# Kernel optimization log

Hardware: AMD Instinct MI355X
Metric: run time of the kernel (lower is better)

Reference implementation:

```python
import jax, jax.numpy as jnp
import numpy as np

N_NODES = 100000
N_EDGES = 1500000
N_REL = 3
HID = 256


def setup_inputs() -> dict:
    key = jax.random.key(0)
    ks = jax.random.split(key, 8)
    return {
        "feat_a": jax.random.normal(ks[0], (N_NODES, 256), dtype=jnp.float32),
        "feat_b": jax.random.normal(ks[1], (N_NODES, 384), dtype=jnp.float32),
        "Wp_a": jax.random.normal(ks[2], (256, HID), dtype=jnp.float32) * 0.03,
        "Wp_b": jax.random.normal(ks[3], (384, HID), dtype=jnp.float32) * 0.03,
        "Wr": jax.random.normal(ks[4], (N_REL, HID, HID), dtype=jnp.float32) * 0.06,
        "ln_gamma": jnp.ones((HID,), dtype=jnp.float32),
        "ln_beta": jnp.zeros((HID,), dtype=jnp.float32),
        "edge_weight": jax.random.uniform(ks[5], (N_EDGES,), dtype=jnp.float32),
        "edge_src": jax.random.randint(ks[6], (N_EDGES,), 0, N_NODES, dtype=jnp.int32),
        "edge_dst": jax.random.randint(ks[7], (N_EDGES,), 0, N_NODES, dtype=jnp.int32),
    }


def _layer_norm(x, gamma, beta, eps=1e-5):
    mu = jnp.mean(x, axis=-1, keepdims=True)
    var = jnp.mean(jnp.square(x - mu), axis=-1, keepdims=True)
    return (x - mu) * jax.lax.rsqrt(var + eps) * gamma + beta


def reference(feat_a, feat_b, Wp_a, Wp_b, Wr, ln_gamma, ln_beta,
              edge_weight, edge_src, edge_dst):
    # avg fusion of modality projections (bias-free linears), padding node zeroed
    h0 = 0.5 * (feat_a @ Wp_a + feat_b @ Wp_b)  # [N, H]
    h0 = h0.at[0].set(0.0)

    n = h0.shape[0]
    e_per_rel = edge_src.shape[0] // N_REL  # edges pre-sorted by relation id
    aggregated = jnp.zeros_like(h0)
    for r in range(N_REL):
        s = slice(r * e_per_rel, (r + 1) * e_per_rel)
        src, dst, w = edge_src[s], edge_dst[s], edge_weight[s]
        # gather -> relation linear -> weight scale  [E_r, H]
        msg = (h0[src] @ Wr[r]) * w[:, None]
        num = jax.ops.segment_sum(msg, dst, num_segments=n)
        den = jax.ops.segment_sum(w, dst, num_segments=n)
        aggregated = aggregated + num / jnp.maximum(den, 1e-8)[:, None]

    # dropout p=0 / eval -> identity; residual + LayerNorm, padding node zeroed
    h1 = _layer_norm(h0 + aggregated, ln_gamma, ln_beta)
    h1 = h1.at[0].set(0.0)
    return h1
```

## Files before the change

### kernel.cpp

```cpp
#include <hip/hip_runtime.h>

#define N_NODES 100000
#define HID 256
#define N_EDGES 1500000
#define N_REL 3
#define E_PER_REL (N_EDGES / N_REL)
#define NKEYS (N_REL * N_NODES)
#define KP 640
#define KR 768

#define SCAN_CHUNK 1024
#define NSCANBLK ((NKEYS + SCAN_CHUNK - 1) / SCAN_CHUNK)

typedef __attribute__((ext_vector_type(8))) short bf16x8;
typedef __attribute__((ext_vector_type(4))) float f32x4;

__device__ __forceinline__ short f2bf(float x) {
    union { float f; unsigned u; } v; v.f = x;
    unsigned r = v.u + 0x7fffu + ((v.u >> 16) & 1u);
    return (short)(r >> 16);
}
__device__ __forceinline__ float bf2f(short h) {
    union { unsigned u; float f; } v;
    v.u = ((unsigned)(unsigned short)h) << 16;
    return v.f;
}
__device__ __forceinline__ int xorf(int r) { return (r & 3) ^ ((r >> 2) & 3); }

__device__ __forceinline__ void gload16(const void* g, void* l) {
    typedef const __attribute__((address_space(1))) unsigned int gq;
    typedef __attribute__((address_space(3))) unsigned int lq;
    __builtin_amdgcn_global_load_lds((gq*)g, (lq*)l, 16, 0, 0);
}

__global__ __launch_bounds__(256) void wprep_kernel(
    const float* __restrict__ Wa, const float* __restrict__ Wb,
    const float* __restrict__ Wr,
    short* __restrict__ WTp, short* __restrict__ WTr)
{
    int idx = blockIdx.x * 256 + threadIdx.x;
    if (idx < 256 * KP) {
        int c = idx / KP, k = idx - c * KP;
        float v = (k < 256) ? Wa[k * HID + c] : Wb[(k - 256) * HID + c];
        WTp[idx] = f2bf(0.5f * v);
    } else {
        int j = idx - 256 * KP;
        if (j < 256 * KR) {
            int c = j / KR, k = j - c * KR;
            WTr[j] = f2bf(Wr[(k >> 8) * HID * HID + (k & 255) * HID + c]);
        }
    }
}

__global__ __launch_bounds__(512, 2) void proj_gemm(
    const float* __restrict__ fa, const float* __restrict__ fb,
    const short* __restrict__ WTp, short* __restrict__ h0h,
    unsigned char* __restrict__ h0q, float* __restrict__ h0scale)
{
    __shared__ alignas(16) char lds[98304];
    const int tid = threadIdx.x;
    const int lane = tid & 63;
    const int w = tid >> 6;
    const int wr = w >> 2, wc = w & 3;
    const int brow = blockIdx.x * 128;

    auto bufA = [&](int b) -> char* { return lds + b * 32768; };
    auto bufB = [&](int b) -> char* { return lds + b * 32768 + 16384; };

    f32x4 acc[4][4] = {};

    const int a_r8 = lane >> 3;
    const int a_sl = (lane & 7) ^ a_r8;
    int aRowG[2];
    #pragma unroll
    for (int ii = 0; ii < 2; ++ii) {
        int i = w * 2 + ii;
        int gr = brow + i * 8 + a_r8;
        aRowG[ii] = (gr < N_NODES) ? gr : (N_NODES - 1);
    }
    const int b_c16 = lane >> 2;
    int bColL[2], bSl[2];
    #pragma unroll
    for (int ii = 0; ii < 2; ++ii) {
        int i = w * 2 + ii;
        bColL[ii] = i * 16 + b_c16;
        bSl[ii] = (lane & 3) ^ xorf(bColL[ii]);
    }

    auto stage = [&](int b, int k0) {
        const float* asrc; int astr, kk;
        if (k0 < 256) { asrc = fa; astr = 256; kk = k0; }
        else          { asrc = fb; astr = 384; kk = k0 - 256; }
        #pragma unroll
        for (int ii = 0; ii < 2; ++ii) {
            int i = w * 2 + ii;
            gload16(asrc + (size_t)aRowG[ii] * astr + kk + a_sl * 4,
                    bufA(b) + i * 1024);
        }
        #pragma unroll
        for (int ii = 0; ii < 2; ++ii) {
            int i = w * 2 + ii;
            gload16(WTp + (size_t)bColL[ii] * KP + k0 + bSl[ii] * 8,
                    bufB(b) + i * 1024);
        }
    };

    const int nt = KP / 32;
    stage(0, 0); stage(1, 32); stage(2, 64);
    int cur = 0;
    for (int t = 0; t < nt; ++t) {
        if (t < nt - 2)       asm volatile("s_waitcnt vmcnt(8)" ::: "memory");
        else if (t == nt - 2) asm volatile("s_waitcnt vmcnt(4)" ::: "memory");
        else                  asm volatile("s_waitcnt vmcnt(0)" ::: "memory");
        __builtin_amdgcn_s_barrier();

        bf16x8 afr[4], bfr[4];
        #pragma unroll
        for (int m = 0; m < 4; ++m) {
            int rt = wr * 64 + m * 16 + (lane & 15);
            int p0 = (((lane >> 4) << 1) | 0) ^ (rt & 7);
            int p1 = (((lane >> 4) << 1) | 1) ^ (rt & 7);
            f32x4 lo = *(const f32x4*)(bufA(cur) + rt * 128 + p0 * 16);
            f32x4 hi = *(const f32x4*)(bufA(cur) + rt * 128 + p1 * 16);
            union { bf16x8 h; unsigned u[4]; } cv;
            asm("v_cvt_pk_bf16_f32 %0, %1, %2" : "=v"(cv.u[0]) : "v"(lo.x), "v"(lo.y));
            asm("v_cvt_pk_bf16_f32 %0, %1, %2" : "=v"(cv.u[1]) : "v"(lo.z), "v"(lo.w));
            asm("v_cvt_pk_bf16_f32 %0, %1, %2" : "=v"(cv.u[2]) : "v"(hi.x), "v"(hi.y));
            asm("v_cvt_pk_bf16_f32 %0, %1, %2" : "=v"(cv.u[3]) : "v"(hi.z), "v"(hi.w));
            afr[m] = cv.h;
        }
        #pragma unroll
        for (int n = 0; n < 4; ++n) {
            int ct = wc * 64 + n * 16 + (lane & 15);
            int p = (lane >> 4) ^ xorf(ct);
            bfr[n] = *(const bf16x8*)(bufB(cur) + ct * 64 + p * 16);
        }
        #pragma unroll
        for (int m = 0; m < 4; ++m)
            #pragma unroll
            for (int n = 0; n < 4; ++n)
                acc[m][n] = __builtin_amdgcn_mfma_f32_16x16x32_bf16(
                    afr[m], bfr[n], acc[m][n], 0, 0, 0);

        asm volatile("s_waitcnt lgkmcnt(0)" ::: "memory");
        __builtin_amdgcn_sched_barrier(0);
        __builtin_amdgcn_s_barrier();
        if (t + 3 < nt) stage(cur, (t + 3) * 32);
        cur = (cur == 2) ? 0 : cur + 1;
    }

    float* redM  = (float*)lds;
    float* smInv = redM + 512;
    #pragma unroll
    for (int m = 0; m < 4; ++m) {
        #pragma unroll
        for (int j = 0; j < 4; ++j) {
            int lrow = wr * 64 + m * 16 + ((lane >> 4) << 2) + j;
            float mx = 0.f;
            #pragma unroll
            for (int n = 0; n < 4; ++n) mx = fmaxf(mx, fabsf(acc[m][n][j]));
            #pragma unroll
            for (int off = 1; off < 16; off <<= 1)
                mx = fmaxf(mx, __shfl_xor(mx, off, 64));
            if ((lane & 15) == 0) redM[lrow * 4 + wc] = mx;
        }
    }
    __syncthreads();
    if (tid < 128) {
        float rm = fmaxf(fmaxf(redM[tid * 4 + 0], redM[tid * 4 + 1]),
                         fmaxf(redM[tid * 4 + 2], redM[tid * 4 + 3]));
        int grow = brow + tid;
        smInv[tid] = (rm > 0.f) ? 127.0f / rm : 0.f;
        if (grow < N_NODES)
            h0scale[grow] = (grow == 0) ? 0.f : rm * (1.0f / 127.0f);
    }
    __syncthreads();

    #pragma unroll
    for (int m = 0; m < 4; ++m) {
        #pragma unroll
        for (int j = 0; j < 4; ++j) {
            int lrow = wr * 64 + m * 16 + ((lane >> 4) << 2) + j;
            int row = brow + lrow;
            if (row >= N_NODES) continue;
            float inv = smInv[lrow];
            #pragma unroll
            for (int n = 0; n < 4; ++n) {
                int col = wc * 64 + n * 16 + (lane & 15);
                float x = acc[m][n][j];
                short v = (row == 0) ? (short)0 : f2bf(x);
                int qi = (row == 0) ? 0 : (int)rintf(x * inv);
                h0h[(size_t)row * HID + col] = v;
                h0q[(size_t)row * HID + col] = (unsigned char)(signed char)qi;
            }
        }
    }
}

__global__ __launch_bounds__(512, 4) void rel_gemm_ln(
    const short* __restrict__ S, const short* __restrict__ WTr,
    const short* __restrict__ h0h,
    const float* __restrict__ gamma, const float* __restrict__ beta,
    float* __restrict__ out)
{
    __shared__ alignas(16) char lds[73728];
    const int tid = threadIdx.x;
    const int lane = tid & 63;
    const int w = tid >> 6;
    const int wr = w >> 2, wc = w & 3;
    const int brow = blockIdx.x * 128;

    auto bufA = [&](int b) -> char* { return lds + b * 24576; };
    auto bufB = [&](int b) -> char* { return lds + b * 24576 + 8192; };

    f32x4 acc[4][4] = {};

    const int s_r16 = lane >> 2;
    const int sRowL = w * 16 + s_r16;
    int gr0 = brow + sRowL;
    const int sRowG = (gr0 < N_NODES) ? gr0 : (N_NODES - 1);
    const int sSl = (lane & 3) ^ xorf(sRowL);
    const int b_c16 = lane >> 2;
    int bColL[2], bSl[2];
    #pragma unroll
    for (int ii = 0; ii < 2; ++ii) {
        int i = w * 2 + ii;
        bColL[ii] = i * 16 + b_c16;
        bSl[ii] = (lane & 3) ^ xorf(bColL[ii]);
    }

    auto stage = [&](int b, int k0) {
        gload16(S + (size_t)sRowG * KR + k0 + sSl * 8, bufA(b) + w * 1024);
        #pragma unroll
        for (int ii = 0; ii < 2; ++ii) {
            int i = w * 2 + ii;
            gload16(WTr + (size_t)bColL[ii] * KR + k0 + bSl[ii] * 8,
                    bufB(b) + i * 1024);
        }
    };

    const int nt = KR / 32;
    stage(0, 0); stage(1, 32); stage(2, 64);
    int cur = 0;
    for (int t = 0; t < nt; ++t) {
        if (t < nt - 2)       asm volatile("s_waitcnt vmcnt(6)" ::: "memory");
        else if (t == nt - 2) asm volatile("s_waitcnt vmcnt(3)" ::: "memory");
        else                  asm volatile("s_waitcnt vmcnt(0)" ::: "memory");
        __builtin_amdgcn_s_barrier();

        bf16x8 afr[4], bfr[4];
        #pragma unroll
        for (int m = 0; m < 4; ++m) {
            int rt = wr * 64 + m * 16 + (lane & 15);
            int p = (lane >> 4) ^ xorf(rt);
            afr[m] = *(const bf16x8*)(bufA(cur) + rt * 64 + p * 16);
        }
        #pragma unroll
        for (int n = 0; n < 4; ++n) {
            int ct = wc * 64 + n * 16 + (lane & 15);
            int p = (lane >> 4) ^ xorf(ct);
            bfr[n] = *(const bf16x8*)(bufB(cur) + ct * 64 + p * 16);
        }
        #pragma unroll
        for (int m = 0; m < 4; ++m)
            #pragma unroll
            for (int n = 0; n < 4; ++n)
                acc[m][n] = __builtin_amdgcn_mfma_f32_16x16x32_bf16(
                    afr[m], bfr[n], acc[m][n], 0, 0, 0);

        asm volatile("s_waitcnt lgkmcnt(0)" ::: "memory");
        __builtin_amdgcn_sched_barrier(0);
        __builtin_amdgcn_s_barrier();
        if (t + 3 < nt) stage(cur, (t + 3) * 32);
        cur = (cur == 2) ? 0 : cur + 1;
    }

    float* redS  = (float*)lds;
    float* redS2 = redS + 512;
    float* smMean = redS2 + 512;
    float* smRs   = smMean + 128;

    float gk[4], bk[4];
    #pragma unroll
    for (int n = 0; n < 4; ++n) {
        int col = wc * 64 + n * 16 + (lane & 15);
        gk[n] = gamma[col];
        bk[n] = beta[col];
    }

    #pragma unroll
    for (int m = 0; m < 4; ++m) {
        #pragma unroll
        for (int j = 0; j < 4; ++j) {
            int lrow = wr * 64 + m * 16 + ((lane >> 4) << 2) + j;
            int grow = brow + lrow;
            int crow = (grow < N_NODES) ? grow : 0;
            float s = 0.f, s2 = 0.f;
            #pragma unroll
            for (int n = 0; n < 4; ++n) {
                int col = wc * 64 + n * 16 + (lane & 15);
                float x = acc[m][n][j] + bf2f(h0h[(size_t)crow * HID + col]);
                acc[m][n][j] = x;
                s += x; s2 = fmaf(x, x, s2);
            }
            #pragma unroll
            for (int off = 1; off < 16; off <<= 1) {
                s += __shfl_xor(s, off, 64);
                s2 += __shfl_xor(s2, off, 64);
            }
            if ((lane & 15) == 0) { redS[lrow * 4 + wc] = s; redS2[lrow * 4 + wc] = s2; }
        }
    }
    __syncthreads();
    if (tid < 128) {
        float tot  = redS[tid * 4 + 0] + redS[tid * 4 + 1] + redS[tid * 4 + 2] + redS[tid * 4 + 3];
        float tot2 = redS2[tid * 4 + 0] + redS2[tid * 4 + 1] + redS2[tid * 4 + 2] + redS2[tid * 4 + 3];
        float mean = tot * (1.0f / HID);
        float var = tot2 * (1.0f / HID) - mean * mean;
        smMean[tid] = mean;
        smRs[tid] = rsqrtf(var + 1e-5f);
    }
    __syncthreads();
    #pragma unroll
    for (int m = 0; m < 4; ++m) {
        #pragma unroll
        for (int j = 0; j < 4; ++j) {
            int lrow = wr * 64 + m * 16 + ((lane >> 4) << 2) + j;
            int grow = brow + lrow;
            if (grow >= N_NODES) continue;
            float mean = smMean[lrow], rs = smRs[lrow];
            #pragma unroll
            for (int n = 0; n < 4; ++n) {
                int col = wc * 64 + n * 16 + (lane & 15);
                float y = (acc[m][n][j] - mean) * rs * gk[n] + bk[n];
                out[(size_t)grow * HID + col] = (grow == 0) ? 0.f : y;
            }
        }
    }
}

__global__ __launch_bounds__(256) void hist_kernel(
    const int* __restrict__ dst, int* __restrict__ count)
{
    int i = blockIdx.x * 256 + threadIdx.x;
    if (i >= N_EDGES) return;
    int r = i / E_PER_REL;
    atomicAdd(&count[r * N_NODES + dst[i]], 1);
}

__global__ __launch_bounds__(256) void scan1_kernel(
    const int* __restrict__ count, int* __restrict__ offset,
    int* __restrict__ bsum)
{
    __shared__ int tmp[256];
    const int t = threadIdx.x;
    const int base = blockIdx.x * SCAN_CHUNK + t * 4;
    int v[4];
    #pragma unroll
    for (int j = 0; j < 4; ++j)
        v[j] = (base + j < NKEYS) ? count[base + j] : 0;
    int tsum = v[0] + v[1] + v[2] + v[3];
    tmp[t] = tsum;
    __syncthreads();
    #pragma unroll
    for (int off = 1; off < 256; off <<= 1) {
        int x = (t >= off) ? tmp[t - off] : 0;
        __syncthreads();
        tmp[t] += x;
        __syncthreads();
    }
    int run = tmp[t] - tsum;
    #pragma unroll
    for (int j = 0; j < 4; ++j) {
        if (base + j < NKEYS) offset[base + j] = run;
        run += v[j];
    }
    if (t == 0) bsum[blockIdx.x] = tmp[255];
}

__global__ __launch_bounds__(256) void scan2_kernel(int* __restrict__ bsum)
{
    __shared__ int tmp[256];
    const int t = threadIdx.x;
    int v0 = (2 * t     < NSCANBLK) ? bsum[2 * t]     : 0;
    int v1 = (2 * t + 1 < NSCANBLK) ? bsum[2 * t + 1] : 0;
    int psum = v0 + v1;
    tmp[t] = psum;
    __syncthreads();
    #pragma unroll
    for (int off = 1; off < 256; off <<= 1) {
        int x = (t >= off) ? tmp[t - off] : 0;
        __syncthreads();
        tmp[t] += x;
        __syncthreads();
    }
    int excl = tmp[t] - psum;
    if (2 * t     < NSCANBLK) bsum[2 * t]     = excl;
    if (2 * t + 1 < NSCANBLK) bsum[2 * t + 1] = excl + v0;
}

__global__ __launch_bounds__(256) void scan3_kernel(
    int* __restrict__ offset, const int* __restrict__ bsum)
{
    int i = blockIdx.x * 256 + threadIdx.x;
    if (i >= NKEYS) return;
    offset[i] += bsum[i / SCAN_CHUNK];
}

__global__ __launch_bounds__(256) void fill_kernel(
    const int* __restrict__ src, const int* __restrict__ dst,
    const float* __restrict__ w, const float* __restrict__ h0scale,
    int* __restrict__ offset, int4* __restrict__ csr4)
{
    int i = blockIdx.x * 256 + threadIdx.x;
    if (i >= N_EDGES) return;
    int r = i / E_PER_REL;
    int key = r * N_NODES + dst[i];
    int pos = atomicAdd(&offset[key], 1);
    int s = src[i];
    float wt = w[i];
    float ws = wt * h0scale[s];
    csr4[pos] = make_int4(s, __float_as_int(wt), __float_as_int(ws), 0);
}

__global__ __launch_bounds__(256) void gather_kernel(
    const unsigned char* __restrict__ h0q,
    const int* __restrict__ ends, const int* __restrict__ count,
    const int4* __restrict__ csr4,
    short* __restrict__ S)
{
    int gw = (blockIdx.x * 256 + threadIdx.x) >> 6;
    int lane = threadIdx.x & 63;
    if (gw >= N_REL * N_NODES) return;
    int r = gw / N_NODES;
    int node = gw - r * N_NODES;
    int deg = count[gw];
    int end = ends[gw];
    int start = end - deg;
    const int colo = lane * 4;

    float a0 = 0.f, a1 = 0.f, a2 = 0.f, a3 = 0.f;
    float den = 0.f;

    if (deg > 0) {
        int degc = (deg < 64) ? deg : 64;
        int4 e = csr4[start + ((lane < degc) ? lane : 0)];
        int msrc = e.x;
        float mw = (lane < degc) ? __int_as_float(e.y) : 0.f;
        int mws = (lane < degc) ? e.z : 0;

        float d = mw;
        #pragma unroll
        for (int off = 1; off < 64; off <<= 1) d += __shfl_xor(d, off, 64);
        den = d;

        int p = 0;
        for (; p + 4 <= degc; p += 4) {
            #pragma unroll
            for (int j = 0; j < 4; ++j) {
                int q = p + j;
                int sj = __builtin_amdgcn_readlane(msrc, q);
                float wsj = __int_as_float(__builtin_amdgcn_readlane(mws, q));
                unsigned qv = *(const unsigned*)(h0q + (size_t)sj * HID + colo);
                a0 = fmaf(wsj, (float)(int)(signed char)(qv & 255u), a0);
                a1 = fmaf(wsj, (float)(int)(signed char)((qv >> 8) & 255u), a1);
                a2 = fmaf(wsj, (float)(int)(signed char)((qv >> 16) & 255u), a2);
                a3 = fmaf(wsj, (float)(int)(signed char)(qv >> 24), a3);
            }
        }
        for (; p < degc; ++p) {
            int sj = __builtin_amdgcn_readlane(msrc, p);
            float wsj = __int_as_float(__builtin_amdgcn_readlane(mws, p));
            unsigned qv = *(const unsigned*)(h0q + (size_t)sj * HID + colo);
            a0 = fmaf(wsj, (float)(int)(signed char)(qv & 255u), a0);
            a1 = fmaf(wsj, (float)(int)(signed char)((qv >> 8) & 255u), a1);
            a2 = fmaf(wsj, (float)(int)(signed char)((qv >> 16) & 255u), a2);
            a3 = fmaf(wsj, (float)(int)(signed char)(qv >> 24), a3);
        }
        for (int pp = start + 64; pp < end; ++pp) {
            int4 ee = csr4[pp];
            float wt = __int_as_float(ee.y);
            float wsj = __int_as_float(ee.z);
            unsigned qv = *(const unsigned*)(h0q + (size_t)ee.x * HID + colo);
            a0 = fmaf(wsj, (float)(int)(signed char)(qv & 255u), a0);
            a1 = fmaf(wsj, (float)(int)(signed char)((qv >> 8) & 255u), a1);
            a2 = fmaf(wsj, (float)(int)(signed char)((qv >> 16) & 255u), a2);
            a3 = fmaf(wsj, (float)(int)(signed char)(qv >> 24), a3);
            den += wt;
        }
    }

    float inv = 1.0f / fmaxf(den, 1e-8f);
    short4 o;
    o.x = f2bf(a0 * inv);
    o.y = f2bf(a1 * inv);
    o.z = f2bf(a2 * inv);
    o.w = f2bf(a3 * inv);
    *(short4*)(S + (size_t)node * KR + r * HID + colo) = o;
}

extern "C" void kernel_launch(void* const* d_in, const int* in_sizes, int n_in,
                              void* d_out, int out_size, void* d_ws, size_t ws_size,
                              hipStream_t stream) {
    const float* fa    = (const float*)d_in[0];
    const float* fb    = (const float*)d_in[1];
    const float* Wa    = (const float*)d_in[2];
    const float* Wb    = (const float*)d_in[3];
    const float* Wr    = (const float*)d_in[4];
    const float* gamma = (const float*)d_in[5];
    const float* beta  = (const float*)d_in[6];
    const float* ew    = (const float*)d_in[7];
    const int*   esrc  = (const int*)d_in[8];
    const int*   edst  = (const int*)d_in[9];
    float* out = (float*)d_out;

    char* ws = (char*)d_ws;
    size_t off = 0;
    short* h0h     = (short*)(ws + off); off += (size_t)N_NODES * HID * 2;
    short* S       = (short*)(ws + off); off += (size_t)N_NODES * KR * 2;
    short* WTp     = (short*)(ws + off); off += (size_t)256 * KP * 2;
    short* WTr     = (short*)(ws + off); off += (size_t)256 * KR * 2;
    int*   count   = (int*)  (ws + off); off += (size_t)NKEYS * 4;
    int*   offs    = (int*)  (ws + off); off += (size_t)NKEYS * 4;
    int*   bsum    = (int*)  (ws + off); off += 4096;
    int4*  csr4    = (int4*) (ws + off); off += (size_t)N_EDGES * 16;
    unsigned char* h0q = (unsigned char*)(ws + off); off += (size_t)N_NODES * HID;
    float* h0scale = (float*)(ws + off); off += (size_t)N_NODES * 4;

    wprep_kernel<<<(256 * KP + 256 * KR) / 256, 256, 0, stream>>>(
        Wa, Wb, Wr, WTp, WTr);

    const int ngrid = (N_NODES + 127) / 128;
    proj_gemm<<<ngrid, 512, 0, stream>>>(fa, fb, WTp, h0h, h0q, h0scale);

    hipMemsetAsync(count, 0, (size_t)NKEYS * 4, stream);
    const int egrid = (N_EDGES + 255) / 256;
    hist_kernel<<<egrid, 256, 0, stream>>>(edst, count);
    scan1_kernel<<<NSCANBLK, 256, 0, stream>>>(count, offs, bsum);
    scan2_kernel<<<1, 256, 0, stream>>>(bsum);
    scan3_kernel<<<(NKEYS + 255) / 256, 256, 0, stream>>>(offs, bsum);
    fill_kernel<<<egrid, 256, 0, stream>>>(esrc, edst, ew, h0scale, offs, csr4);

    gather_kernel<<<(N_REL * N_NODES * 64) / 256, 256, 0, stream>>>(
        h0q, offs, count, csr4, S);

    rel_gemm_ln<<<ngrid, 512, 0, stream>>>(S, WTr, h0h, gamma, beta, out);
}
```

Before: 507.5 us.

## Drop LDS staging in GEMMs and reuse int8 h0 for residual

Both GEMM kernels stop staging tiles through LDS with async global-to-LDS loads and a triple-buffered pipeline. Each lane now loads its MFMA fragments directly from global memory, relying on cache, and the launch bounds of proj_gemm are raised to allow more resident blocks. Separately, the bf16 copy of h0 is no longer written. The LayerNorm residual is rebuilt from the int8-quantized h0 and its per-row scale, which saves a write and a read of a 51 MB array. This brings quantization error into the residual path, and the direct global loads lose the coalescing and overlap the LDS pipeline gave.

```diff
diff --git a/kernel.cpp b/kernel.cpp
--- a/kernel.cpp
+++ b/kernel.cpp
@@ -24,13 +24,6 @@
     union { unsigned u; float f; } v;
     v.u = ((unsigned)(unsigned short)h) << 16;
     return v.f;
-}
-__device__ __forceinline__ int xorf(int r) { return (r & 3) ^ ((r >> 2) & 3); }
-
-__device__ __forceinline__ void gload16(const void* g, void* l) {
-    typedef const __attribute__((address_space(1))) unsigned int gq;
-    typedef __attribute__((address_space(3))) unsigned int lq;
-    __builtin_amdgcn_global_load_lds((gq*)g, (lq*)l, 16, 0, 0);
 }
 
 __global__ __launch_bounds__(256) void wprep_kernel(
@@ -52,76 +45,42 @@
     }
 }
 
-__global__ __launch_bounds__(512, 2) void proj_gemm(
+__global__ __launch_bounds__(512, 4) void proj_gemm(
     const float* __restrict__ fa, const float* __restrict__ fb,
-    const short* __restrict__ WTp, short* __restrict__ h0h,
+    const short* __restrict__ WTp,
     unsigned char* __restrict__ h0q, float* __restrict__ h0scale)
 {
-    __shared__ alignas(16) char lds[98304];
+    __shared__ float redM[128 * 4];
+    __shared__ float smInv[128];
     const int tid = threadIdx.x;
     const int lane = tid & 63;
     const int w = tid >> 6;
     const int wr = w >> 2, wc = w & 3;
     const int brow = blockIdx.x * 128;
 
-    auto bufA = [&](int b) -> char* { return lds + b * 32768; };
-    auto bufB = [&](int b) -> char* { return lds + b * 32768 + 16384; };
-
     f32x4 acc[4][4] = {};
 
-    const int a_r8 = lane >> 3;
-    const int a_sl = (lane & 7) ^ a_r8;
-    int aRowG[2];
-    #pragma unroll
-    for (int ii = 0; ii < 2; ++ii) {
-        int i = w * 2 + ii;
-        int gr = brow + i * 8 + a_r8;
-        aRowG[ii] = (gr < N_NODES) ? gr : (N_NODES - 1);
-    }
-    const int b_c16 = lane >> 2;
-    int bColL[2], bSl[2];
-    #pragma unroll
-    for (int ii = 0; ii < 2; ++ii) {
-        int i = w * 2 + ii;
-        bColL[ii] = i * 16 + b_c16;
-        bSl[ii] = (lane & 3) ^ xorf(bColL[ii]);
-    }
-
-    auto stage = [&](int b, int k0) {
+    int garow[4];
+    #pragma unroll
+    for (int m = 0; m < 4; ++m) {
+        int gr = brow + wr * 64 + m * 16 + (lane & 15);
+        garow[m] = (gr < N_NODES) ? gr : (N_NODES - 1);
+    }
+    const int kq = (lane >> 4) * 8;
+    int bct[4];
+    #pragma unroll
+    for (int n = 0; n < 4; ++n) bct[n] = wc * 64 + n * 16 + (lane & 15);
+
+    for (int k0 = 0; k0 < KP; k0 += 32) {
         const float* asrc; int astr, kk;
         if (k0 < 256) { asrc = fa; astr = 256; kk = k0; }
         else          { asrc = fb; astr = 384; kk = k0 - 256; }
-        #pragma unroll
-        for (int ii = 0; ii < 2; ++ii) {
-            int i = w * 2 + ii;
-            gload16(asrc + (size_t)aRowG[ii] * astr + kk + a_sl * 4,
-                    bufA(b) + i * 1024);
-        }
-        #pragma unroll
-        for (int ii = 0; ii < 2; ++ii) {
-            int i = w * 2 + ii;
-            gload16(WTp + (size_t)bColL[ii] * KP + k0 + bSl[ii] * 8,
-                    bufB(b) + i * 1024);
-        }
-    };
-
-    const int nt = KP / 32;
-    stage(0, 0); stage(1, 32); stage(2, 64);
-    int cur = 0;
-    for (int t = 0; t < nt; ++t) {
-        if (t < nt - 2)       asm volatile("s_waitcnt vmcnt(8)" ::: "memory");
-        else if (t == nt - 2) asm volatile("s_waitcnt vmcnt(4)" ::: "memory");
-        else                  asm volatile("s_waitcnt vmcnt(0)" ::: "memory");
-        __builtin_amdgcn_s_barrier();
-
         bf16x8 afr[4], bfr[4];
         #pragma unroll
         for (int m = 0; m < 4; ++m) {
-            int rt = wr * 64 + m * 16 + (lane & 15);
-            int p0 = (((lane >> 4) << 1) | 0) ^ (rt & 7);
-            int p1 = (((lane >> 4) << 1) | 1) ^ (rt & 7);
-            f32x4 lo = *(const f32x4*)(bufA(cur) + rt * 128 + p0 * 16);
-            f32x4 hi = *(const f32x4*)(bufA(cur) + rt * 128 + p1 * 16);
+            const float* ap = asrc + (size_t)garow[m] * astr + kk + kq;
+            f32x4 lo = *(const f32x4*)(ap + 0);
+            f32x4 hi = *(const f32x4*)(ap + 4);
             union { bf16x8 h; unsigned u[4]; } cv;
             asm("v_cvt_pk_bf16_f32 %0, %1, %2" : "=v"(cv.u[0]) : "v"(lo.x), "v"(lo.y));
             asm("v_cvt_pk_bf16_f32 %0, %1, %2" : "=v"(cv.u[1]) : "v"(lo.z), "v"(lo.w));
@@ -130,27 +89,16 @@
             afr[m] = cv.h;
         }
         #pragma unroll
-        for (int n = 0; n < 4; ++n) {
-            int ct = wc * 64 + n * 16 + (lane & 15);
-            int p = (lane >> 4) ^ xorf(ct);
-            bfr[n] = *(const bf16x8*)(bufB(cur) + ct * 64 + p * 16);
-        }
+        for (int n = 0; n < 4; ++n)
+            bfr[n] = *(const bf16x8*)(WTp + (size_t)bct[n] * KP + k0 + kq);
         #pragma unroll
         for (int m = 0; m < 4; ++m)
             #pragma unroll
             for (int n = 0; n < 4; ++n)
                 acc[m][n] = __builtin_amdgcn_mfma_f32_16x16x32_bf16(
                     afr[m], bfr[n], acc[m][n], 0, 0, 0);
-
-        asm volatile("s_waitcnt lgkmcnt(0)" ::: "memory");
-        __builtin_amdgcn_sched_barrier(0);
-        __builtin_amdgcn_s_barrier();
-        if (t + 3 < nt) stage(cur, (t + 3) * 32);
-        cur = (cur == 2) ? 0 : cur + 1;
-    }
-
-    float* redM  = (float*)lds;
-    float* smInv = redM + 512;
+    }
+
     #pragma unroll
     for (int m = 0; m < 4; ++m) {
         #pragma unroll
@@ -187,10 +135,7 @@
             #pragma unroll
             for (int n = 0; n < 4; ++n) {
                 int col = wc * 64 + n * 16 + (lane & 15);
-                float x = acc[m][n][j];
-                short v = (row == 0) ? (short)0 : f2bf(x);
-                int qi = (row == 0) ? 0 : (int)rintf(x * inv);
-                h0h[(size_t)row * HID + col] = v;
+                int qi = (row == 0) ? 0 : (int)rintf(acc[m][n][j] * inv);
                 h0q[(size_t)row * HID + col] = (unsigned char)(signed char)qi;
             }
         }
@@ -199,86 +144,47 @@
 
 __global__ __launch_bounds__(512, 4) void rel_gemm_ln(
     const short* __restrict__ S, const short* __restrict__ WTr,
-    const short* __restrict__ h0h,
+    const unsigned char* __restrict__ h0q, const float* __restrict__ h0scale,
     const float* __restrict__ gamma, const float* __restrict__ beta,
     float* __restrict__ out)
 {
-    __shared__ alignas(16) char lds[73728];
+    __shared__ float redS[128 * 4];
+    __shared__ float redS2[128 * 4];
+    __shared__ float smMean[128], smRs[128];
     const int tid = threadIdx.x;
     const int lane = tid & 63;
     const int w = tid >> 6;
     const int wr = w >> 2, wc = w & 3;
     const int brow = blockIdx.x * 128;
 
-    auto bufA = [&](int b) -> char* { return lds + b * 24576; };
-    auto bufB = [&](int b) -> char* { return lds + b * 24576 + 8192; };
-
     f32x4 acc[4][4] = {};
 
-    const int s_r16 = lane >> 2;
-    const int sRowL = w * 16 + s_r16;
-    int gr0 = brow + sRowL;
-    const int sRowG = (gr0 < N_NODES) ? gr0 : (N_NODES - 1);
-    const int sSl = (lane & 3) ^ xorf(sRowL);
-    const int b_c16 = lane >> 2;
-    int bColL[2], bSl[2];
-    #pragma unroll
-    for (int ii = 0; ii < 2; ++ii) {
-        int i = w * 2 + ii;
-        bColL[ii] = i * 16 + b_c16;
-        bSl[ii] = (lane & 3) ^ xorf(bColL[ii]);
-    }
-
-    auto stage = [&](int b, int k0) {
-        gload16(S + (size_t)sRowG * KR + k0 + sSl * 8, bufA(b) + w * 1024);
-        #pragma unroll
-        for (int ii = 0; ii < 2; ++ii) {
-            int i = w * 2 + ii;
-            gload16(WTr + (size_t)bColL[ii] * KR + k0 + bSl[ii] * 8,
-                    bufB(b) + i * 1024);
-        }
-    };
-
-    const int nt = KR / 32;
-    stage(0, 0); stage(1, 32); stage(2, 64);
-    int cur = 0;
-    for (int t = 0; t < nt; ++t) {
-        if (t < nt - 2)       asm volatile("s_waitcnt vmcnt(6)" ::: "memory");
-        else if (t == nt - 2) asm volatile("s_waitcnt vmcnt(3)" ::: "memory");
-        else                  asm volatile("s_waitcnt vmcnt(0)" ::: "memory");
-        __builtin_amdgcn_s_barrier();
-
+    int garow[4];
+    #pragma unroll
+    for (int m = 0; m < 4; ++m) {
+        int gr = brow + wr * 64 + m * 16 + (lane & 15);
+        garow[m] = (gr < N_NODES) ? gr : (N_NODES - 1);
+    }
+    const int kq = (lane >> 4) * 8;
+    int bct[4];
+    #pragma unroll
+    for (int n = 0; n < 4; ++n) bct[n] = wc * 64 + n * 16 + (lane & 15);
+
+    for (int k0 = 0; k0 < KR; k0 += 32) {
         bf16x8 afr[4], bfr[4];
         #pragma unroll
-        for (int m = 0; m < 4; ++m) {
-            int rt = wr * 64 + m * 16 + (lane & 15);
-            int p = (lane >> 4) ^ xorf(rt);
-            afr[m] = *(const bf16x8*)(bufA(cur) + rt * 64 + p * 16);
-        }
-        #pragma unroll
-        for (int n = 0; n < 4; ++n) {
-            int ct = wc * 64 + n * 16 + (lane & 15);
-            int p = (lane >> 4) ^ xorf(ct);
-            bfr[n] = *(const bf16x8*)(bufB(cur) + ct * 64 + p * 16);
-        }
+        for (int m = 0; m < 4; ++m)
+            afr[m] = *(const bf16x8*)(S + (size_t)garow[m] * KR + k0 + kq);
+        #pragma unroll
+        for (int n = 0; n < 4; ++n)
+            bfr[n] = *(const bf16x8*)(WTr + (size_t)bct[n] * KR + k0 + kq);
         #pragma unroll
         for (int m = 0; m < 4; ++m)
             #pragma unroll
             for (int n = 0; n < 4; ++n)
                 acc[m][n] = __builtin_amdgcn_mfma_f32_16x16x32_bf16(
                     afr[m], bfr[n], acc[m][n], 0, 0, 0);
-
-        asm volatile("s_waitcnt lgkmcnt(0)" ::: "memory");
-        __builtin_amdgcn_sched_barrier(0);
-        __builtin_amdgcn_s_barrier();
-        if (t + 3 < nt) stage(cur, (t + 3) * 32);
-        cur = (cur == 2) ? 0 : cur + 1;
-    }
-
-    float* redS  = (float*)lds;
-    float* redS2 = redS + 512;
-    float* smMean = redS2 + 512;
-    float* smRs   = smMean + 128;
+    }
 
     float gk[4], bk[4];
     #pragma unroll
@@ -295,11 +201,13 @@
             int lrow = wr * 64 + m * 16 + ((lane >> 4) << 2) + j;
             int grow = brow + lrow;
             int crow = (grow < N_NODES) ? grow : 0;
+            float sc = h0scale[crow];
             float s = 0.f, s2 = 0.f;
             #pragma unroll
             for (int n = 0; n < 4; ++n) {
                 int col = wc * 64 + n * 16 + (lane & 15);
-                float x = acc[m][n][j] + bf2f(h0h[(size_t)crow * HID + col]);
+                float hq = (float)(int)(signed char)h0q[(size_t)crow * HID + col];
+                float x = acc[m][n][j] + hq * sc;
                 acc[m][n][j] = x;
                 s += x; s2 = fmaf(x, x, s2);
             }
@@ -516,7 +424,6 @@
 
     char* ws = (char*)d_ws;
     size_t off = 0;
-    short* h0h     = (short*)(ws + off); off += (size_t)N_NODES * HID * 2;
     short* S       = (short*)(ws + off); off += (size_t)N_NODES * KR * 2;
     short* WTp     = (short*)(ws + off); off += (size_t)256 * KP * 2;
     short* WTr     = (short*)(ws + off); off += (size_t)256 * KR * 2;
@@ -531,7 +438,7 @@
         Wa, Wb, Wr, WTp, WTr);
 
     const int ngrid = (N_NODES + 127) / 128;
-    proj_gemm<<<ngrid, 512, 0, stream>>>(fa, fb, WTp, h0h, h0q, h0scale);
+    proj_gemm<<<ngrid, 512, 0, stream>>>(fa, fb, WTp, h0q, h0scale);
 
     hipMemsetAsync(count, 0, (size_t)NKEYS * 4, stream);
     const int egrid = (N_EDGES + 255) / 256;
@@ -544,5 +451,5 @@
     gather_kernel<<<(N_REL * N_NODES * 64) / 256, 256, 0, stream>>>(
         h0q, offs, count, csr4, S);
 
-    rel_gemm_ln<<<ngrid, 512, 0, stream>>>(S, WTr, h0h, gamma, beta, out);
-}
+    rel_gemm_ln<<<ngrid, 512, 0, stream>>>(S, WTr, h0q, h0scale, gamma, beta, out);
+}
```

Measured after the change: 740.1 us. +45.8%, slower.
